# Performance work log

Hardware: AMD Instinct MI355X
Metric: run time of the kernel (lower is better)

The kernel has to match this reference:

```python
import jax, jax.numpy as jnp
import numpy as np
from jax.ops import segment_sum, segment_max

G_GRAPHS = 64  # number of graphs for global_mean_pool
H_ATTN = 4     # GPSConv global attention heads


def _bn(h, g, b, eps=1e-5):
    # BatchNorm1d over nodes, training-mode (biased) batch statistics
    mu = h.mean(0)
    var = ((h - mu) ** 2).mean(0)
    return (h - mu) * jax.lax.rsqrt(var + eps) * g + b


def _forward(x, edge_index, batch, pre_w1, pre_b1, pre_w2, pre_b2,
             gat_wl, gat_bl, gat_wr, gat_br, gat_att, gat_bias,
             attn_in_w, attn_in_b, attn_out_w, attn_out_b,
             bn1_g, bn1_b, bn2_g, bn2_b, bn3_g, bn3_b,
             mlp_w1, mlp_b1, mlp_w2, mlp_b2, fin_w, fin_b):
    N = x.shape[0]
    L = gat_wl.shape[0]
    loops = jnp.arange(N)
    src = jnp.concatenate([edge_index[0], loops])  # GATv2Conv add_self_loops=True
    dst = jnp.concatenate([edge_index[1], loops])

    # preprocess MLP (exact GELU, as torch.nn.GELU default)
    x = jax.nn.gelu(x @ pre_w1 + pre_b1, approximate=False)
    x = jax.nn.gelu(x @ pre_w2 + pre_b2, approximate=False)

    for l in range(L):
        D = x.shape[1]
        dh = D // H_ATTN
        # ---- local GATv2Conv (heads=1, concat) ----
        xl = x @ gat_wl[l] + gat_bl[l]  # source transform
        xr = x @ gat_wr[l] + gat_br[l]  # target transform
        e = jax.nn.leaky_relu(xl[src] + xr[dst], 0.2) @ gat_att[l]  # [E]
        m = segment_max(e, dst, num_segments=N)
        a = jnp.exp(e - m[dst])
        s = segment_sum(a, dst, num_segments=N)
        alpha = a / s[dst]
        h1 = segment_sum(alpha[:, None] * xl[src], dst, num_segments=N) + gat_bias[l]
        h1 = _bn(h1 + x, bn1_g[l], bn1_b[l])  # residual + norm1
        # ---- global multi-head self-attention over all N nodes (batch=None) ----
        qkv = x @ attn_in_w[l].T + attn_in_b[l]
        q, k, v = jnp.split(qkv, 3, axis=-1)
        q = q.reshape(N, H_ATTN, dh).transpose(1, 0, 2)  # [H,N,dh]
        k = k.reshape(N, H_ATTN, dh).transpose(1, 0, 2)
        v = v.reshape(N, H_ATTN, dh).transpose(1, 0, 2)
        probs = jax.nn.softmax(jnp.einsum('hnd,hmd->hnm', q, k) / np.sqrt(dh), axis=-1)
        o = jnp.einsum('hnm,hmd->hnd', probs, v).transpose(1, 0, 2).reshape(N, D)
        h2 = o @ attn_out_w[l].T + attn_out_b[l]
        h2 = _bn(h2 + x, bn2_g[l], bn2_b[l])  # residual + norm2
        # ---- combine + MLP + norm3 ----
        out = h1 + h2
        out = out + (jax.nn.relu(out @ mlp_w1[l] + mlp_b1[l]) @ mlp_w2[l] + mlp_b2[l])
        out = _bn(out, bn3_g[l], bn3_b[l])
        x = jax.nn.relu(out)  # outer F.relu; dropout is identity in eval

    # global_mean_pool
    sums = segment_sum(x, batch, num_segments=G_GRAPHS)
    cnt = jnp.maximum(segment_sum(jnp.ones((N,), x.dtype), batch, num_segments=G_GRAPHS), 1.0)
    logits = (sums / cnt[:, None]) @ fin_w + fin_b
    return jax.nn.log_softmax(logits, axis=-1)


def setup_inputs() -> dict:
    N, E, F_IN, D, C, L = 4096, 262144, 9, 64, 10, 3
    key = jax.random.key(0)
    ks = iter(jax.random.split(key, 64))
    def nrm(shape, fan):
        return jax.random.normal(next(ks), shape, jnp.float32) / np.sqrt(fan)
    def zeros(shape):
        return jnp.zeros(shape, jnp.float32)
    x = jax.random.normal(next(ks), (N, F_IN), jnp.float32)
    edge_index = jax.random.randint(next(ks), (2, E), 0, N)
    batch = jnp.sort(jax.random.randint(next(ks), (N,), 0, G_GRAPHS))
    return dict(
        x=x, edge_index=edge_index, batch=batch,
        pre_w1=nrm((F_IN, 2 * D), F_IN), pre_b1=zeros((2 * D,)),
        pre_w2=nrm((2 * D, D), 2 * D), pre_b2=zeros((D,)),
        gat_wl=nrm((L, D, D), D), gat_bl=zeros((L, D)),
        gat_wr=nrm((L, D, D), D), gat_br=zeros((L, D)),
        gat_att=nrm((L, D), D), gat_bias=zeros((L, D)),
        attn_in_w=nrm((L, 3 * D, D), D), attn_in_b=zeros((L, 3 * D)),
        attn_out_w=nrm((L, D, D), D), attn_out_b=zeros((L, D)),
        bn1_g=jnp.ones((L, D), jnp.float32), bn1_b=zeros((L, D)),
        bn2_g=jnp.ones((L, D), jnp.float32), bn2_b=zeros((L, D)),
        bn3_g=jnp.ones((L, D), jnp.float32), bn3_b=zeros((L, D)),
        mlp_w1=nrm((L, D, 2 * D), D), mlp_b1=zeros((L, 2 * D)),
        mlp_w2=nrm((L, 2 * D, D), 2 * D), mlp_b2=zeros((L, D)),
        fin_w=nrm((D, C), D), fin_b=zeros((C,)),
    )


def reference(x, edge_index, batch, pre_w1, pre_b1, pre_w2, pre_b2,
              gat_wl, gat_bl, gat_wr, gat_br, gat_att, gat_bias,
              attn_in_w, attn_in_b, attn_out_w, attn_out_b,
              bn1_g, bn1_b, bn2_g, bn2_b, bn3_g, bn3_b,
              mlp_w1, mlp_b1, mlp_w2, mlp_b2, fin_w, fin_b):
    return _forward(x, edge_index, batch, pre_w1, pre_b1, pre_w2, pre_b2,
                    gat_wl, gat_bl, gat_wr, gat_br, gat_att, gat_bias,
                    attn_in_w, attn_in_b, attn_out_w, attn_out_b,
                    bn1_g, bn1_b, bn2_g, bn2_b, bn3_g, bn3_b,
                    mlp_w1, mlp_b1, mlp_w2, mlp_b2, fin_w, fin_b)
```

## Files before the change

kernel.cpp:

```cpp
#include <hip/hip_runtime.h>
#include <math.h>

#define N_NODE 4096
#define N_EDGE 262144
#define E_TOT (N_EDGE + N_NODE)
#define DD 64
#define NL 3
#define NG 64

__device__ __forceinline__ void atomAddF(float* p, float v) {
#if defined(__HIP_PLATFORM_AMD__)
  unsafeAtomicAdd(p, v);
#else
  atomicAdd(p, v);
#endif
}

__global__ void csr_count_kernel(const int* __restrict__ ei, int* __restrict__ cnt) {
  int e = blockIdx.x * blockDim.x + threadIdx.x;
  if (e >= E_TOT) return;
  int dst = (e < N_EDGE) ? ei[N_EDGE + e] : (e - N_EDGE);
  atomicAdd(&cnt[dst], 1);
}

__global__ void csr_scan_kernel(const int* __restrict__ cnt, int* __restrict__ row_ptr,
                                int* __restrict__ nextp) {
  __shared__ int ps[256];
  __shared__ int ps2[257];
  int t = threadIdx.x;
  int base = t * 16;
  int loc[16];
  int s = 0;
#pragma unroll
  for (int k = 0; k < 16; ++k) { loc[k] = s; s += cnt[base + k]; }
  ps[t] = s;
  __syncthreads();
  if (t == 0) {
    int a = 0;
    for (int u = 0; u < 256; ++u) { ps2[u] = a; a += ps[u]; }
    ps2[256] = a;
  }
  __syncthreads();
  int off = ps2[t];
#pragma unroll
  for (int k = 0; k < 16; ++k) {
    int v = off + loc[k];
    row_ptr[base + k] = v;
    nextp[base + k] = v;
  }
  if (t == 0) row_ptr[N_NODE] = ps2[256];
}

__global__ void csr_fill_kernel(const int* __restrict__ ei, int* __restrict__ nextp,
                                int* __restrict__ csr_src) {
  int e = blockIdx.x * blockDim.x + threadIdx.x;
  if (e >= E_TOT) return;
  int src, dst;
  if (e < N_EDGE) { src = ei[e]; dst = ei[N_EDGE + e]; }
  else { src = dst = e - N_EDGE; }
  int pos = atomicAdd(&nextp[dst], 1);
  csr_src[pos] = src;
}

__global__ void transpose_w_kernel(const float* __restrict__ win, const float* __restrict__ wout,
                                   float* __restrict__ tin, float* __restrict__ tout) {
  int idx = blockIdx.x * blockDim.x + threadIdx.x;
  if (idx < NL * 192 * 64) {
    int l = idx / (192 * 64), rem = idx % (192 * 64);
    int j = rem / 64, k = rem % 64;
    tin[l * 192 * 64 + k * 192 + j] = win[idx];
  }
  if (idx < NL * 64 * 64) {
    int l = idx / 4096, rem = idx % 4096;
    int j = rem / 64, k = rem % 64;
    tout[l * 4096 + k * 64 + j] = wout[idx];
  }
}

__global__ void linear_kernel(const float* __restrict__ A, const float* __restrict__ W,
                              const float* __restrict__ bias, float* __restrict__ C,
                              const float* __restrict__ resid,
                              int K, int Nc, int act) {
  extern __shared__ float sA[];
  int R = blockDim.x / Nc;
  int r = threadIdx.x / Nc;
  int j = threadIdx.x - r * Nc;
  int row0 = blockIdx.x * R;
  for (int idx = threadIdx.x; idx < R * K; idx += blockDim.x)
    sA[idx] = A[row0 * K + idx];
  __syncthreads();
  int row = row0 + r;
  const float* a = sA + r * K;
  float acc = bias[j];
#pragma unroll 8
  for (int k = 0; k < K; ++k) acc = fmaf(a[k], W[k * Nc + j], acc);
  if (act == 1) acc = 0.5f * acc * (1.0f + erff(acc * 0.70710678118654752f));
  else if (act == 2) acc = fmaxf(acc, 0.0f);
  if (resid) acc += resid[row * Nc + j];
  C[row * Nc + j] = acc;
}

__global__ void gat_agg_kernel(const float* __restrict__ x, const float* __restrict__ xl,
                               const float* __restrict__ xr, const float* __restrict__ att,
                               const float* __restrict__ gbias,
                               const int* __restrict__ row_ptr, const int* __restrict__ csr_src,
                               float* __restrict__ z1) {
  int wave = (blockIdx.x * blockDim.x + threadIdx.x) >> 6;
  int lane = threadIdx.x & 63;
  if (wave >= N_NODE) return;
  int i = wave;
  float xr_d = xr[i * DD + lane];
  float att_d = att[lane];
  float m = -INFINITY, s = 0.f, acc = 0.f;
  int e0 = row_ptr[i], e1 = row_ptr[i + 1];
  for (int e = e0; e < e1; ++e) {
    int src = csr_src[e];
    float xl_d = xl[src * DD + lane];
    float v = xl_d + xr_d;
    float lr = (v > 0.f) ? v : 0.2f * v;
    float p = lr * att_d;
#pragma unroll
    for (int off = 32; off; off >>= 1) p += __shfl_xor(p, off, 64);
    float nm = fmaxf(m, p);
    float corr = __expf(m - nm);
    float w = __expf(p - nm);
    s = s * corr + w;
    acc = acc * corr + w * xl_d;
    m = nm;
  }
  z1[i * DD + lane] = x[i * DD + lane] + gbias[lane] + acc / s;
}

__global__ void colstats_kernel(const float* __restrict__ z, float* __restrict__ stats) {
  int d = threadIdx.x & 63;
  int rg = threadIdx.x >> 6;
  int i0 = blockIdx.x * 128;
  float s = 0.f, q = 0.f;
  for (int i = i0 + rg; i < i0 + 128; i += 4) {
    float v = z[i * DD + d];
    s += v;
    q += v * v;
  }
  atomAddF(&stats[d], s);
  atomAddF(&stats[64 + d], q);
}

__global__ void bn_apply_kernel(const float* __restrict__ z, const float* __restrict__ stats,
                                const float* __restrict__ g, const float* __restrict__ b,
                                const float* __restrict__ postadd, float* __restrict__ out,
                                int relu) {
  int idx = blockIdx.x * blockDim.x + threadIdx.x;
  if (idx >= N_NODE * DD) return;
  int d = idx & 63;
  const float invN = 1.0f / (float)N_NODE;
  float mu = stats[d] * invN;
  float var = stats[64 + d] * invN - mu * mu;
  float rstd = rsqrtf(var + 1e-5f);
  float v = (z[idx] - mu) * rstd * g[d] + b[d];
  if (postadd) v += postadd[idx];
  if (relu) v = fmaxf(v, 0.f);
  out[idx] = v;
}

__global__ void knorm_kernel(const float* __restrict__ qkv, int* __restrict__ kmax) {
  __shared__ int lmax[4];
  int tid = threadIdx.x;
  if (tid < 4) lmax[tid] = 0;
  __syncthreads();
  int idx = blockIdx.x * 256 + tid;
  int j = idx >> 2, h = idx & 3;
  const float* kr = qkv + (size_t)j * 192 + 64 + h * 16;
  float n2 = 0.f;
#pragma unroll
  for (int c = 0; c < 16; ++c) { float v = kr[c]; n2 = fmaf(v, v, n2); }
  atomicMax(&lmax[h], __float_as_int(sqrtf(n2)));
  __syncthreads();
  if (tid < 4) atomicMax(&kmax[tid], lmax[tid]);
}

#define TJ 256
__global__ void attn_kernel(const float* __restrict__ qkv, const int* __restrict__ kmax,
                            float* __restrict__ accS, float* __restrict__ accO) {
  __shared__ __align__(16) float kv[TJ * 32];
  int h = blockIdx.y;
  int js = blockIdx.z;
  int i0 = blockIdx.x * 64;
  int r = threadIdx.x & 63;
  int gq = threadIdx.x >> 6;
  int i = i0 + r;
  float q[16];
#pragma unroll
  for (int c = 0; c < 16; ++c) q[c] = qkv[(size_t)i * 192 + h * 16 + c] * 0.25f;
  float qn2 = 0.f;
#pragma unroll
  for (int c = 0; c < 16; ++c) qn2 = fmaf(q[c], q[c], qn2);
  float m = sqrtf(qn2) * __int_as_float(kmax[h]);
  float s = 0.f;
  float acc[16];
#pragma unroll
  for (int c = 0; c < 16; ++c) acc[c] = 0.f;

  for (int t = 0; t < 4; ++t) {
    int j0 = js * 1024 + t * TJ;
    __syncthreads();
    {
      int jj = threadIdx.x;
      const float* kr = qkv + (size_t)(j0 + jj) * 192 + 64 + h * 16;
      const float* vr = qkv + (size_t)(j0 + jj) * 192 + 128 + h * 16;
#pragma unroll
      for (int c = 0; c < 16; c += 4) {
        *(float4*)&kv[jj * 16 + c] = *(const float4*)&kr[c];
        *(float4*)&kv[TJ * 16 + jj * 16 + c] = *(const float4*)&vr[c];
      }
    }
    __syncthreads();
    for (int jt = gq; jt < TJ; jt += 4) {
      const float4* kk = (const float4*)&kv[jt * 16];
      float4 k0 = kk[0], k1 = kk[1], k2 = kk[2], k3 = kk[3];
      float s0 = q[0] * k0.x + q[1] * k0.y + q[2] * k0.z + q[3] * k0.w;
      float s1 = q[4] * k1.x + q[5] * k1.y + q[6] * k1.z + q[7] * k1.w;
      float s2 = q[8] * k2.x + q[9] * k2.y + q[10] * k2.z + q[11] * k2.w;
      float s3 = q[12] * k3.x + q[13] * k3.y + q[14] * k3.z + q[15] * k3.w;
      float p = __expf((s0 + s1) + (s2 + s3) - m);
      const float4* vv = (const float4*)&kv[TJ * 16 + jt * 16];
      float4 v0 = vv[0], v1 = vv[1], v2 = vv[2], v3 = vv[3];
      s += p;
      acc[0] = fmaf(p, v0.x, acc[0]);  acc[1] = fmaf(p, v0.y, acc[1]);
      acc[2] = fmaf(p, v0.z, acc[2]);  acc[3] = fmaf(p, v0.w, acc[3]);
      acc[4] = fmaf(p, v1.x, acc[4]);  acc[5] = fmaf(p, v1.y, acc[5]);
      acc[6] = fmaf(p, v1.z, acc[6]);  acc[7] = fmaf(p, v1.w, acc[7]);
      acc[8] = fmaf(p, v2.x, acc[8]);  acc[9] = fmaf(p, v2.y, acc[9]);
      acc[10] = fmaf(p, v2.z, acc[10]); acc[11] = fmaf(p, v2.w, acc[11]);
      acc[12] = fmaf(p, v3.x, acc[12]); acc[13] = fmaf(p, v3.y, acc[13]);
      acc[14] = fmaf(p, v3.z, acc[14]); acc[15] = fmaf(p, v3.w, acc[15]);
    }
  }
  __syncthreads();
  float* cb = kv;
  cb[(gq * 17 + 16) * 64 + r] = s;
#pragma unroll
  for (int c = 0; c < 16; ++c) cb[(gq * 17 + c) * 64 + r] = acc[c];
  __syncthreads();
  if (gq == 0) {
    float S = 0.f;
#pragma unroll
    for (int g2 = 0; g2 < 4; ++g2) S += cb[(g2 * 17 + 16) * 64 + r];
    atomAddF(&accS[h * N_NODE + i], S);
#pragma unroll
    for (int c = 0; c < 16; ++c) {
      float A = 0.f;
#pragma unroll
      for (int g2 = 0; g2 < 4; ++g2) A += cb[(g2 * 17 + c) * 64 + r];
      atomAddF(&accO[(h * 16 + c) * N_NODE + i], A);
    }
  }
}

__global__ void attn_norm_kernel(const float* __restrict__ accO, const float* __restrict__ accS,
                                 float* __restrict__ o) {
  int idx = blockIdx.x * 256 + threadIdx.x;
  int i = idx >> 6, d = idx & 63, h = d >> 4;
  o[idx] = accO[d * N_NODE + i] / accS[h * N_NODE + i];
}

__global__ void pool_kernel(const float* __restrict__ x, const int* __restrict__ batch,
                            float* __restrict__ pool, float* __restrict__ pcnt) {
  int idx = blockIdx.x * blockDim.x + threadIdx.x;
  if (idx >= N_NODE * DD) return;
  int i = idx >> 6, d = idx & 63;
  int g = batch[i];
  atomAddF(&pool[g * DD + d], x[idx]);
  if (d == 0) atomAddF(&pcnt[g], 1.0f);
}

__global__ void final_kernel(const float* __restrict__ pool, const float* __restrict__ pcnt,
                             const float* __restrict__ fw, const float* __restrict__ fb,
                             float* __restrict__ out) {
  int g = blockIdx.x;
  int d = threadIdx.x;
  __shared__ float mean[64];
  __shared__ float lg[16];
  float c = fmaxf(pcnt[g], 1.0f);
  mean[d] = pool[g * DD + d] / c;
  __syncthreads();
  if (d < 10) {
    float acc = fb[d];
#pragma unroll 8
    for (int k = 0; k < 64; ++k) acc += mean[k] * fw[k * 10 + d];
    lg[d] = acc;
  }
  __syncthreads();
  if (d == 0) {
    float mx = -INFINITY;
    for (int c2 = 0; c2 < 10; ++c2) mx = fmaxf(mx, lg[c2]);
    float sum = 0.f;
    for (int c2 = 0; c2 < 10; ++c2) sum += expf(lg[c2] - mx);
    lg[10] = mx + logf(sum);
  }
  __syncthreads();
  if (d < 10) out[g * 10 + d] = lg[d] - lg[10];
}

static void run_linear(const float* A, const float* W, const float* b, float* C,
                       const float* resid, int K, int Nc, int act, hipStream_t s) {
  int R = (Nc == 64) ? 4 : 2;
  int block = Nc * R;
  int grid = N_NODE / R;
  hipLaunchKernelGGL(linear_kernel, dim3(grid), dim3(block), R * K * sizeof(float), s,
                     A, W, b, C, resid, K, Nc, act);
}

extern "C" void kernel_launch(void* const* d_in, const int* in_sizes, int n_in,
                              void* d_out, int out_size, void* d_ws, size_t ws_size,
                              hipStream_t stream) {
  const float* x_in      = (const float*)d_in[0];
  const int*   edge_idx  = (const int*)d_in[1];
  const int*   batch     = (const int*)d_in[2];
  const float* pre_w1    = (const float*)d_in[3];
  const float* pre_b1    = (const float*)d_in[4];
  const float* pre_w2    = (const float*)d_in[5];
  const float* pre_b2    = (const float*)d_in[6];
  const float* gat_wl    = (const float*)d_in[7];
  const float* gat_bl    = (const float*)d_in[8];
  const float* gat_wr    = (const float*)d_in[9];
  const float* gat_br    = (const float*)d_in[10];
  const float* gat_att   = (const float*)d_in[11];
  const float* gat_bias  = (const float*)d_in[12];
  const float* attn_in_w = (const float*)d_in[13];
  const float* attn_in_b = (const float*)d_in[14];
  const float* attn_out_w= (const float*)d_in[15];
  const float* attn_out_b= (const float*)d_in[16];
  const float* bn1_g     = (const float*)d_in[17];
  const float* bn1_b     = (const float*)d_in[18];
  const float* bn2_g     = (const float*)d_in[19];
  const float* bn2_b     = (const float*)d_in[20];
  const float* bn3_g     = (const float*)d_in[21];
  const float* bn3_b     = (const float*)d_in[22];
  const float* mlp_w1    = (const float*)d_in[23];
  const float* mlp_b1    = (const float*)d_in[24];
  const float* mlp_w2    = (const float*)d_in[25];
  const float* mlp_b2    = (const float*)d_in[26];
  const float* fin_w     = (const float*)d_in[27];
  const float* fin_b     = (const float*)d_in[28];
  float* out = (float*)d_out;

  float* ws = (float*)d_ws;
  float* xbuf  = ws;
  float* xlbuf = xbuf  + N_NODE * DD;
  float* xrbuf = xlbuf + N_NODE * DD;
  float* z1    = xrbuf + N_NODE * DD;
  float* h1n   = z1    + N_NODE * DD;
  float* qkv   = h1n   + N_NODE * DD;
  float* hid   = qkv   + N_NODE * 192;
  float* tin   = hid   + N_NODE * 128;
  float* tout  = tin   + NL * 192 * 64;
  float* zr    = tout  + NL * 64 * 64;
  int*   cnt   = (int*)zr;
  float* stats = zr + 4096;
  float* pool  = stats + 9 * 128;
  float* pcnt  = pool + NG * DD;
  int*   kmax  = (int*)(pcnt + NG);
  float* accS  = (float*)(kmax + 4);
  float* accO  = accS + 4 * N_NODE;
  size_t zr_elems = 4096 + 1152 + 4096 + 64 + 4 + 16384 + 262144;
  float* zend   = accO + 64 * N_NODE;
  int* row_ptr = (int*)zend;
  int* nextp   = row_ptr + N_NODE + 1;
  int* csr_src = nextp + N_NODE;

  hipMemsetAsync(zr, 0, zr_elems * sizeof(float), stream);

  hipLaunchKernelGGL(csr_count_kernel, dim3((E_TOT + 255) / 256), dim3(256), 0, stream,
                     edge_idx, cnt);
  hipLaunchKernelGGL(csr_scan_kernel, dim3(1), dim3(256), 0, stream, cnt, row_ptr, nextp);
  hipLaunchKernelGGL(csr_fill_kernel, dim3((E_TOT + 255) / 256), dim3(256), 0, stream,
                     edge_idx, nextp, csr_src);

  hipLaunchKernelGGL(transpose_w_kernel, dim3((NL * 192 * 64 + 255) / 256), dim3(256), 0, stream,
                     attn_in_w, attn_out_w, tin, tout);

  run_linear(x_in, pre_w1, pre_b1, hid, nullptr, 9, 128, 1, stream);
  run_linear(hid, pre_w2, pre_b2, xbuf, nullptr, 128, 64, 1, stream);

  for (int l = 0; l < NL; ++l) {
    const float* Wl = gat_wl + l * DD * DD;
    const float* bl = gat_bl + l * DD;
    const float* Wr = gat_wr + l * DD * DD;
    const float* br = gat_br + l * DD;
    const float* attv = gat_att + l * DD;
    const float* gbias = gat_bias + l * DD;
    const float* tinl = tin + l * 192 * 64;
    const float* toutl = tout + l * 64 * 64;
    float* st1 = stats + (l * 3 + 0) * 128;
    float* st2 = stats + (l * 3 + 1) * 128;
    float* st3 = stats + (l * 3 + 2) * 128;

    run_linear(xbuf, Wl, bl, xlbuf, nullptr, 64, 64, 0, stream);
    run_linear(xbuf, Wr, br, xrbuf, nullptr, 64, 64, 0, stream);
    hipLaunchKernelGGL(gat_agg_kernel, dim3(N_NODE / 4), dim3(256), 0, stream,
                       xbuf, xlbuf, xrbuf, attv, gbias, row_ptr, csr_src, z1);
    hipLaunchKernelGGL(colstats_kernel, dim3(32), dim3(256), 0, stream, z1, st1);
    hipLaunchKernelGGL(bn_apply_kernel, dim3(N_NODE * DD / 256), dim3(256), 0, stream,
                       z1, st1, bn1_g + l * DD, bn1_b + l * DD, (const float*)nullptr, h1n, 0);

    run_linear(xbuf, tinl, attn_in_b + l * 192, qkv, nullptr, 64, 192, 0, stream);
    hipLaunchKernelGGL(knorm_kernel, dim3(64), dim3(256), 0, stream, qkv, kmax + 0);
    hipLaunchKernelGGL(attn_kernel, dim3(N_NODE / 64, 4, 4), dim3(256), 0, stream,
                       qkv, kmax, accS, accO);
    hipLaunchKernelGGL(attn_norm_kernel, dim3(N_NODE * DD / 256), dim3(256), 0, stream,
                       accO, accS, xlbuf);
    if (l + 1 < NL) {
      hipMemsetAsync(kmax, 0, (4 + 4 * N_NODE + 64 * N_NODE) * sizeof(float) + 0, stream);
    }
    run_linear(xlbuf, toutl, attn_out_b + l * DD, xrbuf, xbuf, 64, 64, 0, stream);
    hipLaunchKernelGGL(colstats_kernel, dim3(32), dim3(256), 0, stream, xrbuf, st2);
    hipLaunchKernelGGL(bn_apply_kernel, dim3(N_NODE * DD / 256), dim3(256), 0, stream,
                       xrbuf, st2, bn2_g + l * DD, bn2_b + l * DD, h1n, z1, 0);

    run_linear(z1, mlp_w1 + l * 64 * 128, mlp_b1 + l * 128, hid, nullptr, 64, 128, 2, stream);
    run_linear(hid, mlp_w2 + l * 128 * 64, mlp_b2 + l * DD, xrbuf, z1, 128, 64, 0, stream);
    hipLaunchKernelGGL(colstats_kernel, dim3(32), dim3(256), 0, stream, xrbuf, st3);
    hipLaunchKernelGGL(bn_apply_kernel, dim3(N_NODE * DD / 256), dim3(256), 0, stream,
                       xrbuf, st3, bn3_g + l * DD, bn3_b + l * DD, (const float*)nullptr, xbuf, 1);
  }

  hipLaunchKernelGGL(pool_kernel, dim3(N_NODE * DD / 256), dim3(256), 0, stream,
                     xbuf, batch, pool, pcnt);
  hipLaunchKernelGGL(final_kernel, dim3(NG), dim3(64), 0, stream, pool, pcnt, fin_w, fin_b, out);
}
```

Baseline: 909.4 us.

## Use packed fp16 dot products in attention and fuse projections and BN kernels

The global attention kernel now converts Q, K and V to packed half precision and uses fdot2 for both the QK scores and the PV accumulation. Pairs of V rows are interleaved so each fdot2 handles two keys at once, and the key range is split across 8 chunks instead of 4. GAT xl/xr and the QKV projection are merged into one 320-column linear launch using a combined weight matrix. The two BN applies for the GAT and attention branches are fused into one kernel. The per-layer memset is replaced by zeroing the accumulators inside attn_norm_kernel. Together these cut ALU work and kernel launches, at the cost of fp16 rounding in the attention scores and weighted sums.

New measurement: 769.8 us. 1.18x faster.

```diff
diff --git a/kernel.cpp b/kernel.cpp
--- a/kernel.cpp
+++ b/kernel.cpp
@@ -7,6 +7,9 @@
 #define DD 64
 #define NL 3
 #define NG 64
+
+typedef __fp16 h2_t __attribute__((ext_vector_type(2)));
+union H2x4 { uint4 u; h2_t h[4]; };
 
 __device__ __forceinline__ void atomAddF(float* p, float v) {
 #if defined(__HIP_PLATFORM_AMD__)
@@ -62,23 +65,40 @@
   csr_src[pos] = src;
 }
 
-__global__ void transpose_w_kernel(const float* __restrict__ win, const float* __restrict__ wout,
-                                   float* __restrict__ tin, float* __restrict__ tout) {
+__global__ void build_w_kernel(const float* __restrict__ wl, const float* __restrict__ bl,
+                               const float* __restrict__ wr, const float* __restrict__ br,
+                               const float* __restrict__ win, const float* __restrict__ bin,
+                               const float* __restrict__ wout,
+                               float* __restrict__ cw, float* __restrict__ cbias,
+                               float* __restrict__ tout) {
   int idx = blockIdx.x * blockDim.x + threadIdx.x;
-  if (idx < NL * 192 * 64) {
-    int l = idx / (192 * 64), rem = idx % (192 * 64);
-    int j = rem / 64, k = rem % 64;
-    tin[l * 192 * 64 + k * 192 + j] = win[idx];
-  }
-  if (idx < NL * 64 * 64) {
+  if (idx < NL * 64 * 320) {
+    int l = idx / 20480, rem = idx % 20480;
+    int k = rem / 320, j = rem % 320;
+    float v;
+    if (j < 64) v = wl[l * 4096 + k * 64 + j];
+    else if (j < 128) v = wr[l * 4096 + k * 64 + (j - 64)];
+    else v = win[l * 12288 + (j - 128) * 64 + k];
+    cw[idx] = v;
+  }
+  if (idx < NL * 320) {
+    int l = idx / 320, j = idx % 320;
+    float v;
+    if (j < 64) v = bl[l * 64 + j];
+    else if (j < 128) v = br[l * 64 + (j - 64)];
+    else v = bin[l * 192 + (j - 128)];
+    cbias[idx] = v;
+  }
+  if (idx < NL * 4096) {
     int l = idx / 4096, rem = idx % 4096;
-    int j = rem / 64, k = rem % 64;
-    tout[l * 4096 + k * 64 + j] = wout[idx];
+    int k = rem / 64, j = rem % 64;
+    tout[l * 4096 + k * 64 + j] = wout[l * 4096 + j * 64 + k];
   }
 }
 
 __global__ void linear_kernel(const float* __restrict__ A, const float* __restrict__ W,
                               const float* __restrict__ bias, float* __restrict__ C,
+                              float* __restrict__ C2, int split,
                               const float* __restrict__ resid,
                               int K, int Nc, int act) {
   extern __shared__ float sA[];
@@ -97,25 +117,25 @@
   if (act == 1) acc = 0.5f * acc * (1.0f + erff(acc * 0.70710678118654752f));
   else if (act == 2) acc = fmaxf(acc, 0.0f);
   if (resid) acc += resid[row * Nc + j];
-  C[row * Nc + j] = acc;
-}
-
-__global__ void gat_agg_kernel(const float* __restrict__ x, const float* __restrict__ xl,
-                               const float* __restrict__ xr, const float* __restrict__ att,
-                               const float* __restrict__ gbias,
+  if (j < split) C[row * split + j] = acc;
+  else C2[row * (Nc - split) + (j - split)] = acc;
+}
+
+__global__ void gat_agg_kernel(const float* __restrict__ x, const float* __restrict__ xlr,
+                               const float* __restrict__ att, const float* __restrict__ gbias,
                                const int* __restrict__ row_ptr, const int* __restrict__ csr_src,
                                float* __restrict__ z1) {
   int wave = (blockIdx.x * blockDim.x + threadIdx.x) >> 6;
   int lane = threadIdx.x & 63;
   if (wave >= N_NODE) return;
   int i = wave;
-  float xr_d = xr[i * DD + lane];
+  float xr_d = xlr[i * 128 + 64 + lane];
   float att_d = att[lane];
   float m = -INFINITY, s = 0.f, acc = 0.f;
   int e0 = row_ptr[i], e1 = row_ptr[i + 1];
   for (int e = e0; e < e1; ++e) {
     int src = csr_src[e];
-    float xl_d = xl[src * DD + lane];
+    float xl_d = xlr[src * 128 + lane];
     float v = xl_d + xr_d;
     float lr = (v > 0.f) ? v : 0.2f * v;
     float p = lr * att_d;
@@ -147,8 +167,7 @@
 
 __global__ void bn_apply_kernel(const float* __restrict__ z, const float* __restrict__ stats,
                                 const float* __restrict__ g, const float* __restrict__ b,
-                                const float* __restrict__ postadd, float* __restrict__ out,
-                                int relu) {
+                                float* __restrict__ out, int relu) {
   int idx = blockIdx.x * blockDim.x + threadIdx.x;
   if (idx >= N_NODE * DD) return;
   int d = idx & 63;
@@ -157,9 +176,26 @@
   float var = stats[64 + d] * invN - mu * mu;
   float rstd = rsqrtf(var + 1e-5f);
   float v = (z[idx] - mu) * rstd * g[d] + b[d];
-  if (postadd) v += postadd[idx];
   if (relu) v = fmaxf(v, 0.f);
   out[idx] = v;
+}
+
+__global__ void bnbn_kernel(const float* __restrict__ z1, const float* __restrict__ st1,
+                            const float* __restrict__ g1, const float* __restrict__ b1,
+                            const float* __restrict__ z2, const float* __restrict__ st2,
+                            const float* __restrict__ g2, const float* __restrict__ b2,
+                            float* __restrict__ comb) {
+  int idx = blockIdx.x * blockDim.x + threadIdx.x;
+  if (idx >= N_NODE * DD) return;
+  int d = idx & 63;
+  const float invN = 1.0f / (float)N_NODE;
+  float mu1 = st1[d] * invN;
+  float v1 = st1[64 + d] * invN - mu1 * mu1;
+  float h1 = (z1[idx] - mu1) * rsqrtf(v1 + 1e-5f) * g1[d] + b1[d];
+  float mu2 = st2[d] * invN;
+  float v2 = st2[64 + d] * invN - mu2 * mu2;
+  float h2 = (z2[idx] - mu2) * rsqrtf(v2 + 1e-5f) * g2[d] + b2[d];
+  comb[idx] = h1 + h2;
 }
 
 __global__ void knorm_kernel(const float* __restrict__ qkv, int* __restrict__ kmax) {
@@ -181,62 +217,86 @@
 #define TJ 256
 __global__ void attn_kernel(const float* __restrict__ qkv, const int* __restrict__ kmax,
                             float* __restrict__ accS, float* __restrict__ accO) {
-  __shared__ __align__(16) float kv[TJ * 32];
-  int h = blockIdx.y;
-  int js = blockIdx.z;
+  __shared__ __align__(16) float smem[4416];
+  uint4* kt = (uint4*)smem;
+  uint4* vt = (uint4*)(smem + 2048);
+  int h = blockIdx.y, js = blockIdx.z;
   int i0 = blockIdx.x * 64;
   int r = threadIdx.x & 63;
   int gq = threadIdx.x >> 6;
   int i = i0 + r;
-  float q[16];
-#pragma unroll
-  for (int c = 0; c < 16; ++c) q[c] = qkv[(size_t)i * 192 + h * 16 + c] * 0.25f;
+  float qf[16];
+  const float* qr = qkv + (size_t)i * 192 + h * 16;
+#pragma unroll
+  for (int c = 0; c < 16; ++c) qf[c] = qr[c] * 0.25f;
   float qn2 = 0.f;
 #pragma unroll
-  for (int c = 0; c < 16; ++c) qn2 = fmaf(q[c], q[c], qn2);
+  for (int c = 0; c < 16; ++c) qn2 = fmaf(qf[c], qf[c], qn2);
   float m = sqrtf(qn2) * __int_as_float(kmax[h]);
+  h2_t q2[8];
+#pragma unroll
+  for (int c = 0; c < 8; ++c) q2[c] = __builtin_amdgcn_cvt_pkrtz(qf[2 * c], qf[2 * c + 1]);
   float s = 0.f;
   float acc[16];
 #pragma unroll
   for (int c = 0; c < 16; ++c) acc[c] = 0.f;
 
-  for (int t = 0; t < 4; ++t) {
-    int j0 = js * 1024 + t * TJ;
+  for (int t = 0; t < 2; ++t) {
+    int j0 = js * 512 + t * TJ;
     __syncthreads();
     {
       int jj = threadIdx.x;
       const float* kr = qkv + (size_t)(j0 + jj) * 192 + 64 + h * 16;
-      const float* vr = qkv + (size_t)(j0 + jj) * 192 + 128 + h * 16;
-#pragma unroll
-      for (int c = 0; c < 16; c += 4) {
-        *(float4*)&kv[jj * 16 + c] = *(const float4*)&kr[c];
-        *(float4*)&kv[TJ * 16 + jj * 16 + c] = *(const float4*)&vr[c];
+      float4 a = *(const float4*)kr, b = *(const float4*)(kr + 4);
+      float4 c4f = *(const float4*)(kr + 8), d4 = *(const float4*)(kr + 12);
+      H2x4 w0, w1;
+      w0.h[0] = __builtin_amdgcn_cvt_pkrtz(a.x, a.y); w0.h[1] = __builtin_amdgcn_cvt_pkrtz(a.z, a.w);
+      w0.h[2] = __builtin_amdgcn_cvt_pkrtz(b.x, b.y); w0.h[3] = __builtin_amdgcn_cvt_pkrtz(b.z, b.w);
+      w1.h[0] = __builtin_amdgcn_cvt_pkrtz(c4f.x, c4f.y); w1.h[1] = __builtin_amdgcn_cvt_pkrtz(c4f.z, c4f.w);
+      w1.h[2] = __builtin_amdgcn_cvt_pkrtz(d4.x, d4.y); w1.h[3] = __builtin_amdgcn_cvt_pkrtz(d4.z, d4.w);
+      kt[jj * 2] = w0.u; kt[jj * 2 + 1] = w1.u;
+      for (int id = threadIdx.x; id < 512; id += 256) {
+        int c4 = id & 3, jp = id >> 2;
+        const float* va = qkv + (size_t)(j0 + 2 * jp) * 192 + 128 + h * 16 + c4 * 4;
+        float4 A = *(const float4*)va, B = *(const float4*)(va + 192);
+        H2x4 w;
+        w.h[0] = __builtin_amdgcn_cvt_pkrtz(A.x, B.x); w.h[1] = __builtin_amdgcn_cvt_pkrtz(A.y, B.y);
+        w.h[2] = __builtin_amdgcn_cvt_pkrtz(A.z, B.z); w.h[3] = __builtin_amdgcn_cvt_pkrtz(A.w, B.w);
+        vt[c4 * 128 + jp] = w.u;
       }
     }
     __syncthreads();
-    for (int jt = gq; jt < TJ; jt += 4) {
-      const float4* kk = (const float4*)&kv[jt * 16];
-      float4 k0 = kk[0], k1 = kk[1], k2 = kk[2], k3 = kk[3];
-      float s0 = q[0] * k0.x + q[1] * k0.y + q[2] * k0.z + q[3] * k0.w;
-      float s1 = q[4] * k1.x + q[5] * k1.y + q[6] * k1.z + q[7] * k1.w;
-      float s2 = q[8] * k2.x + q[9] * k2.y + q[10] * k2.z + q[11] * k2.w;
-      float s3 = q[12] * k3.x + q[13] * k3.y + q[14] * k3.z + q[15] * k3.w;
-      float p = __expf((s0 + s1) + (s2 + s3) - m);
-      const float4* vv = (const float4*)&kv[TJ * 16 + jt * 16];
-      float4 v0 = vv[0], v1 = vv[1], v2 = vv[2], v3 = vv[3];
-      s += p;
-      acc[0] = fmaf(p, v0.x, acc[0]);  acc[1] = fmaf(p, v0.y, acc[1]);
-      acc[2] = fmaf(p, v0.z, acc[2]);  acc[3] = fmaf(p, v0.w, acc[3]);
-      acc[4] = fmaf(p, v1.x, acc[4]);  acc[5] = fmaf(p, v1.y, acc[5]);
-      acc[6] = fmaf(p, v1.z, acc[6]);  acc[7] = fmaf(p, v1.w, acc[7]);
-      acc[8] = fmaf(p, v2.x, acc[8]);  acc[9] = fmaf(p, v2.y, acc[9]);
-      acc[10] = fmaf(p, v2.z, acc[10]); acc[11] = fmaf(p, v2.w, acc[11]);
-      acc[12] = fmaf(p, v3.x, acc[12]); acc[13] = fmaf(p, v3.y, acc[13]);
-      acc[14] = fmaf(p, v3.z, acc[14]); acc[15] = fmaf(p, v3.w, acc[15]);
+    for (int jp = gq; jp < 128; jp += 4) {
+      H2x4 ka0, ka1, kb0, kb1;
+      ka0.u = kt[jp * 4 + 0]; ka1.u = kt[jp * 4 + 1];
+      kb0.u = kt[jp * 4 + 2]; kb1.u = kt[jp * 4 + 3];
+      float sa = 0.f, sb = 0.f;
+#pragma unroll
+      for (int c = 0; c < 4; ++c) {
+        sa = __builtin_amdgcn_fdot2(q2[c], ka0.h[c], sa, false);
+        sb = __builtin_amdgcn_fdot2(q2[c], kb0.h[c], sb, false);
+      }
+#pragma unroll
+      for (int c = 0; c < 4; ++c) {
+        sa = __builtin_amdgcn_fdot2(q2[4 + c], ka1.h[c], sa, false);
+        sb = __builtin_amdgcn_fdot2(q2[4 + c], kb1.h[c], sb, false);
+      }
+      float pa = __expf(sa - m), pb = __expf(sb - m);
+      s += pa + pb;
+      h2_t pp = __builtin_amdgcn_cvt_pkrtz(pa, pb);
+      H2x4 v0, v1, v2, v3;
+      v0.u = vt[jp]; v1.u = vt[128 + jp]; v2.u = vt[256 + jp]; v3.u = vt[384 + jp];
+#pragma unroll
+      for (int c = 0; c < 4; ++c) {
+        acc[c]      = __builtin_amdgcn_fdot2(pp, v0.h[c], acc[c], false);
+        acc[4 + c]  = __builtin_amdgcn_fdot2(pp, v1.h[c], acc[4 + c], false);
+        acc[8 + c]  = __builtin_amdgcn_fdot2(pp, v2.h[c], acc[8 + c], false);
+        acc[12 + c] = __builtin_amdgcn_fdot2(pp, v3.h[c], acc[12 + c], false);
+      }
     }
   }
   __syncthreads();
-  float* cb = kv;
+  float* cb = smem;
   cb[(gq * 17 + 16) * 64 + r] = s;
 #pragma unroll
   for (int c = 0; c < 16; ++c) cb[(gq * 17 + c) * 64 + r] = acc[c];
@@ -256,11 +316,15 @@
   }
 }
 
-__global__ void attn_norm_kernel(const float* __restrict__ accO, const float* __restrict__ accS,
-                                 float* __restrict__ o) {
+__global__ void attn_norm_kernel(float* __restrict__ accO, float* __restrict__ accS,
+                                 int* __restrict__ kmax, float* __restrict__ o) {
   int idx = blockIdx.x * 256 + threadIdx.x;
   int i = idx >> 6, d = idx & 63, h = d >> 4;
   o[idx] = accO[d * N_NODE + i] / accS[h * N_NODE + i];
+  __syncthreads();
+  accO[d * N_NODE + i] = 0.f;
+  if ((d & 15) == 0) accS[h * N_NODE + i] = 0.f;
+  if (idx < 4) kmax[idx] = 0;
 }
 
 __global__ void pool_kernel(const float* __restrict__ x, const int* __restrict__ batch,
@@ -302,12 +366,12 @@
 }
 
 static void run_linear(const float* A, const float* W, const float* b, float* C,
-                       const float* resid, int K, int Nc, int act, hipStream_t s) {
-  int R = (Nc == 64) ? 4 : 2;
+                       float* C2, int split, const float* resid,
+                       int K, int Nc, int act, int R, hipStream_t s) {
   int block = Nc * R;
   int grid = N_NODE / R;
   hipLaunchKernelGGL(linear_kernel, dim3(grid), dim3(block), R * K * sizeof(float), s,
-                     A, W, b, C, resid, K, Nc, act);
+                     A, W, b, C, C2, split, resid, K, Nc, act);
 }
 
 extern "C" void kernel_launch(void* const* d_in, const int* in_sizes, int n_in,
@@ -346,27 +410,29 @@
 
   float* ws = (float*)d_ws;
   float* xbuf  = ws;
-  float* xlbuf = xbuf  + N_NODE * DD;
-  float* xrbuf = xlbuf + N_NODE * DD;
-  float* z1    = xrbuf + N_NODE * DD;
-  float* h1n   = z1    + N_NODE * DD;
-  float* qkv   = h1n   + N_NODE * DD;
-  float* hid   = qkv   + N_NODE * 192;
-  float* tin   = hid   + N_NODE * 128;
-  float* tout  = tin   + NL * 192 * 64;
-  float* zr    = tout  + NL * 64 * 64;
+  float* qkv   = xbuf + 262144;
+  float* xlr   = qkv + 786432;
+  float* hid   = xlr + 524288;
+  float* obuf  = hid;
+  float* z1    = hid + 262144;
+  float* z2    = hid + 524288;
+  float* comb  = z2 + 262144;
+  float* cw    = comb + 262144;
+  float* cbias = cw + 61440;
+  float* tout  = cbias + 960;
+  float* zr    = tout + 12288;
   int*   cnt   = (int*)zr;
   float* stats = zr + 4096;
-  float* pool  = stats + 9 * 128;
-  float* pcnt  = pool + NG * DD;
-  int*   kmax  = (int*)(pcnt + NG);
+  float* pool  = stats + 1152;
+  float* pcnt  = pool + 4096;
+  int*   kmax  = (int*)(pcnt + 64);
   float* accS  = (float*)(kmax + 4);
-  float* accO  = accS + 4 * N_NODE;
+  float* accO  = accS + 16384;
   size_t zr_elems = 4096 + 1152 + 4096 + 64 + 4 + 16384 + 262144;
-  float* zend   = accO + 64 * N_NODE;
+  float* zend  = accO + 262144;
   int* row_ptr = (int*)zend;
-  int* nextp   = row_ptr + N_NODE + 1;
-  int* csr_src = nextp + N_NODE;
+  int* nextp   = row_ptr + 4097;
+  int* csr_src = nextp + 4096;
 
   hipMemsetAsync(zr, 0, zr_elems * sizeof(float), stream);
 
@@ -376,52 +442,48 @@
   hipLaunchKernelGGL(csr_fill_kernel, dim3((E_TOT + 255) / 256), dim3(256), 0, stream,
                      edge_idx, nextp, csr_src);
 
-  hipLaunchKernelGGL(transpose_w_kernel, dim3((NL * 192 * 64 + 255) / 256), dim3(256), 0, stream,
-                     attn_in_w, attn_out_w, tin, tout);
-
-  run_linear(x_in, pre_w1, pre_b1, hid, nullptr, 9, 128, 1, stream);
-  run_linear(hid, pre_w2, pre_b2, xbuf, nullptr, 128, 64, 1, stream);
+  hipLaunchKernelGGL(build_w_kernel, dim3((NL * 64 * 320 + 255) / 256), dim3(256), 0, stream,
+                     gat_wl, gat_bl, gat_wr, gat_br, attn_in_w, attn_in_b, attn_out_w,
+                     cw, cbias, tout);
+
+  run_linear(x_in, pre_w1, pre_b1, xlr, nullptr, 128, nullptr, 9, 128, 1, 2, stream);
+  run_linear(xlr, pre_w2, pre_b2, xbuf, nullptr, 64, nullptr, 128, 64, 1, 4, stream);
 
   for (int l = 0; l < NL; ++l) {
-    const float* Wl = gat_wl + l * DD * DD;
-    const float* bl = gat_bl + l * DD;
-    const float* Wr = gat_wr + l * DD * DD;
-    const float* br = gat_br + l * DD;
     const float* attv = gat_att + l * DD;
     const float* gbias = gat_bias + l * DD;
-    const float* tinl = tin + l * 192 * 64;
-    const float* toutl = tout + l * 64 * 64;
     float* st1 = stats + (l * 3 + 0) * 128;
     float* st2 = stats + (l * 3 + 1) * 128;
     float* st3 = stats + (l * 3 + 2) * 128;
 
-    run_linear(xbuf, Wl, bl, xlbuf, nullptr, 64, 64, 0, stream);
-    run_linear(xbuf, Wr, br, xrbuf, nullptr, 64, 64, 0, stream);
-    hipLaunchKernelGGL(gat_agg_kernel, dim3(N_NODE / 4), dim3(256), 0, stream,
-                       xbuf, xlbuf, xrbuf, attv, gbias, row_ptr, csr_src, z1);
-    hipLaunchKernelGGL(colstats_kernel, dim3(32), dim3(256), 0, stream, z1, st1);
-    hipLaunchKernelGGL(bn_apply_kernel, dim3(N_NODE * DD / 256), dim3(256), 0, stream,
-                       z1, st1, bn1_g + l * DD, bn1_b + l * DD, (const float*)nullptr, h1n, 0);
-
-    run_linear(xbuf, tinl, attn_in_b + l * 192, qkv, nullptr, 64, 192, 0, stream);
-    hipLaunchKernelGGL(knorm_kernel, dim3(64), dim3(256), 0, stream, qkv, kmax + 0);
-    hipLaunchKernelGGL(attn_kernel, dim3(N_NODE / 64, 4, 4), dim3(256), 0, stream,
+    run_linear(xbuf, cw + l * 20480, cbias + l * 320, xlr, qkv, 128, nullptr,
+               64, 320, 0, 2, stream);
+
+    hipLaunchKernelGGL(knorm_kernel, dim3(64), dim3(256), 0, stream, qkv, kmax);
+    hipLaunchKernelGGL(attn_kernel, dim3(N_NODE / 64, 4, 8), dim3(256), 0, stream,
                        qkv, kmax, accS, accO);
     hipLaunchKernelGGL(attn_norm_kernel, dim3(N_NODE * DD / 256), dim3(256), 0, stream,
-                       accO, accS, xlbuf);
-    if (l + 1 < NL) {
-      hipMemsetAsync(kmax, 0, (4 + 4 * N_NODE + 64 * N_NODE) * sizeof(float) + 0, stream);
-    }
-    run_linear(xlbuf, toutl, attn_out_b + l * DD, xrbuf, xbuf, 64, 64, 0, stream);
-    hipLaunchKernelGGL(colstats_kernel, dim3(32), dim3(256), 0, stream, xrbuf, st2);
+                       accO, accS, kmax, obuf);
+
+    hipLaunchKernelGGL(gat_agg_kernel, dim3(N_NODE / 4), dim3(256), 0, stream,
+                       xbuf, xlr, attv, gbias, row_ptr, csr_src, z1);
+    hipLaunchKernelGGL(colstats_kernel, dim3(32), dim3(256), 0, stream, z1, st1);
+
+    run_linear(obuf, tout + l * 4096, attn_out_b + l * DD, z2, nullptr, 64, xbuf,
+               64, 64, 0, 4, stream);
+    hipLaunchKernelGGL(colstats_kernel, dim3(32), dim3(256), 0, stream, z2, st2);
+
+    hipLaunchKernelGGL(bnbn_kernel, dim3(N_NODE * DD / 256), dim3(256), 0, stream,
+                       z1, st1, bn1_g + l * DD, bn1_b + l * DD,
+                       z2, st2, bn2_g + l * DD, bn2_b + l * DD, comb);
+
+    run_linear(comb, mlp_w1 + l * 8192, mlp_b1 + l * 128, hid, nullptr, 128, nullptr,
+               64, 128, 2, 2, stream);
+    run_linear(hid, mlp_w2 + l * 8192, mlp_b2 + l * DD, z2, nullptr, 64, comb,
+               128, 64, 0, 4, stream);
+    hipLaunchKernelGGL(colstats_kernel, dim3(32), dim3(256), 0, stream, z2, st3);
     hipLaunchKernelGGL(bn_apply_kernel, dim3(N_NODE * DD / 256), dim3(256), 0, stream,
-                       xrbuf, st2, bn2_g + l * DD, bn2_b + l * DD, h1n, z1, 0);
-
-    run_linear(z1, mlp_w1 + l * 64 * 128, mlp_b1 + l * 128, hid, nullptr, 64, 128, 2, stream);
-    run_linear(hid, mlp_w2 + l * 128 * 64, mlp_b2 + l * DD, xrbuf, z1, 128, 64, 0, stream);
-    hipLaunchKernelGGL(colstats_kernel, dim3(32), dim3(256), 0, stream, xrbuf, st3);
-    hipLaunchKernelGGL(bn_apply_kernel, dim3(N_NODE * DD / 256), dim3(256), 0, stream,
-                       xrbuf, st3, bn3_g + l * DD, bn3_b + l * DD, (const float*)nullptr, xbuf, 1);
+                       z2, st3, bn3_g + l * DD, bn3_b + l * DD, xbuf, 1);
   }
 
   hipLaunchKernelGGL(pool_kernel, dim3(N_NODE * DD / 256), dim3(256), 0, stream,
```
